# Optimization experiments

Measured on AMD Instinct MI355X. Metric: run time of the kernel, lower is better.

Reference implementation:

```python
import jax, jax.numpy as jnp
import numpy as np

E, T, A, H = 64, 128, 32, 4
S, O, QH1, QD, C1 = 256, 128, 128, 64, 128  # state, obs, query hidden, query/key dim, c hidden


def setup_inputs() -> dict:
    key = jax.random.key(0)
    ks = jax.random.split(key, 10)
    w = 0.02
    return {
        "q_values": jax.random.normal(ks[0], (E, T, A), jnp.float32),
        "states": jax.random.normal(ks[1], (E, T, S), jnp.float32),
        "individual_fs": jax.random.normal(ks[2], (E, T, A, O), jnp.float32),
        "Wq1": jax.random.normal(ks[3], (S, QH1), jnp.float32) * w,
        "bq1": jnp.zeros((QH1,), jnp.float32),
        "Wq2": jax.random.normal(ks[4], (QH1, QD), jnp.float32) * w,
        "bq2": jnp.zeros((QD,), jnp.float32),
        "Wk": jax.random.normal(ks[5], (H, O, QD), jnp.float32) * w,
        "bk": jnp.zeros((H, QD), jnp.float32),
        "Wc1": jax.random.normal(ks[6], (S, C1), jnp.float32) * w,
        "bc1": jnp.zeros((C1,), jnp.float32),
        "Wc2": jax.random.normal(ks[7], (C1, 1), jnp.float32) * w,
        "bc2": jnp.zeros((1,), jnp.float32),
    }


def reference(q_values, states, individual_fs, Wq1, bq1, Wq2, bq2, Wk, bk, Wc1, bc1, Wc2, bc2):
    e, t, a = q_values.shape
    s = states.reshape(-1, states.shape[-1])              # (B, S), B = E*T
    f = individual_fs.reshape(e * t, a, -1)               # (B, A, O)
    # query embedding of state: 2-layer MLP with ReLU
    emb_s = jnp.maximum(s @ Wq1 + bq1, 0.0) @ Wq2 + bq2   # (B, QD)
    # all-agents, all-heads key extraction in one batched einsum
    emb_u = jnp.einsum('bao,hok->bahk', f, Wk) + bk       # (B, A, H, QD)
    # query-key dot products per agent/head, then sum over heads
    Lambda_i = jnp.einsum('bk,bahk->bah', emb_s, emb_u).sum(axis=-1)  # (B, A)
    # state-dependent scalar bias
    c_value = jnp.maximum(s @ Wc1 + bc1, 0.0) @ Wc2 + bc2  # (B, 1)
    Q_tot = jnp.sum(Lambda_i * q_values.reshape(-1, a), axis=-1, keepdims=True) + c_value
    return Q_tot.reshape(e, t, 1)
```

## Files before the change

kernel.cpp:

```cpp
#include <hip/hip_runtime.h>


static constexpr int Sd  = 256;
static constexpr int Ad  = 32;
static constexpr int Od  = 128;
static constexpr int QDd = 64;
static constexpr int NB  = 16;
static constexpr int A_BLOCKS = 512;
static constexpr int B_BLOCKS = 1024;

__global__ void qatten_prep(const float* __restrict__ Wk, const float* __restrict__ bk,
                            float* __restrict__ WkT, float* __restrict__ bkSum)
{
    int idx = blockIdx.x * 256 + threadIdx.x;
    int k = idx >> 7;
    int o = idx & 127;
    float s = 0.f;
#pragma unroll
    for (int h = 0; h < 4; ++h) s += Wk[h * (Od * QDd) + o * QDd + k];
    WkT[k * Od + o] = s;
    if (idx < QDd) {
        float t = 0.f;
#pragma unroll
        for (int h = 0; h < 4; ++h) t += bk[h * QDd + idx];
        bkSum[idx] = t;
    }
}

__global__ __launch_bounds__(256, 4) void qatten_main(
    const float* __restrict__ qv, const float* __restrict__ st, const float* __restrict__ fs,
    const float* __restrict__ Wq1, const float* __restrict__ bq1,
    const float* __restrict__ Wq2, const float* __restrict__ bq2,
    const float* __restrict__ Wc1, const float* __restrict__ bc1,
    const float* __restrict__ Wc2, const float* __restrict__ bc2,
    const float* __restrict__ WkT, const float* __restrict__ bkSum,
    float* __restrict__ v_out, float* __restrict__ bias_out, float* __restrict__ g_out)
{
    __shared__ float s_lds[NB][Sd];
    __shared__ float h_lds[NB][260];
    __shared__ float emb_lds[NB][68];

    const int tid = threadIdx.x;
    const int bid = blockIdx.x;

    if (bid < A_BLOCKS) {
        const int b0 = bid * NB;

        {
            const float4* sp = (const float4*)(st + (size_t)b0 * Sd);
            float4* sl = (float4*)&s_lds[0][0];
            sl[tid]       = sp[tid];
            sl[tid + 256] = sp[tid + 256];
            sl[tid + 512] = sp[tid + 512];
            sl[tid + 768] = sp[tid + 768];
        }
        __syncthreads();

        {
            const int wg = tid & 63;
            const int rg = (tid >> 6) << 2;
            const float* __restrict__ Wb = (wg < 32) ? (Wq1 + 4 * wg)
                                                     : (Wc1 + 4 * (wg - 32));
            const float4 bb4 = (wg < 32) ? *(const float4*)&bq1[4 * wg]
                                         : *(const float4*)&bc1[4 * (wg - 32)];
            float acc[4][4];
#pragma unroll
            for (int r = 0; r < 4; ++r)
#pragma unroll
                for (int c = 0; c < 4; ++c) acc[r][c] = 0.f;

            for (int k = 0; k < Sd; k += 4) {
                float w[4][4], sv[4][4];
#pragma unroll
                for (int kk = 0; kk < 4; ++kk) {
                    const float4 t = *(const float4*)&Wb[(size_t)(k + kk) * 128];
                    w[kk][0] = t.x; w[kk][1] = t.y; w[kk][2] = t.z; w[kk][3] = t.w;
                }
#pragma unroll
                for (int r = 0; r < 4; ++r) {
                    const float4 t = *(const float4*)&s_lds[rg + r][k];
                    sv[r][0] = t.x; sv[r][1] = t.y; sv[r][2] = t.z; sv[r][3] = t.w;
                }
#pragma unroll
                for (int r = 0; r < 4; ++r)
#pragma unroll
                    for (int kk = 0; kk < 4; ++kk)
#pragma unroll
                        for (int c = 0; c < 4; ++c)
                            acc[r][c] = fmaf(sv[r][kk], w[kk][c], acc[r][c]);
            }
#pragma unroll
            for (int r = 0; r < 4; ++r) {
                float4 o;
                o.x = fmaxf(acc[r][0] + bb4.x, 0.f);
                o.y = fmaxf(acc[r][1] + bb4.y, 0.f);
                o.z = fmaxf(acc[r][2] + bb4.z, 0.f);
                o.w = fmaxf(acc[r][3] + bb4.w, 0.f);
                *(float4*)&h_lds[rg + r][4 * wg] = o;
            }
        }
        __syncthreads();

        {
            const int cg = tid & 15;
            const int row = tid >> 4;
            float acc[4] = {0.f, 0.f, 0.f, 0.f};
            for (int k = 0; k < 128; k += 4) {
                float w[4][4];
#pragma unroll
                for (int kk = 0; kk < 4; ++kk) {
                    const float4 t = *(const float4*)&Wq2[(size_t)(k + kk) * 64 + 4 * cg];
                    w[kk][0] = t.x; w[kk][1] = t.y; w[kk][2] = t.z; w[kk][3] = t.w;
                }
                const float4 h4 = *(const float4*)&h_lds[row][k];
                float hv[4] = {h4.x, h4.y, h4.z, h4.w};
#pragma unroll
                for (int kk = 0; kk < 4; ++kk)
#pragma unroll
                    for (int c = 0; c < 4; ++c)
                        acc[c] = fmaf(hv[kk], w[kk][c], acc[c]);
            }
            const float4 b4 = *(const float4*)&bq2[4 * cg];
            float4 o;
            o.x = acc[0] + b4.x; o.y = acc[1] + b4.y;
            o.z = acc[2] + b4.z; o.w = acc[3] + b4.w;
            *(float4*)&emb_lds[row][4 * cg] = o;
        }
        __syncthreads();

        {
            const int cg = tid & 31;
            const int rp = (tid >> 5) << 1;
            float acc[2][4];
#pragma unroll
            for (int r = 0; r < 2; ++r)
#pragma unroll
                for (int c = 0; c < 4; ++c) acc[r][c] = 0.f;
            for (int k = 0; k < QDd; k += 4) {
                float w[4][4], ev[2][4];
#pragma unroll
                for (int kk = 0; kk < 4; ++kk) {
                    const float4 t = *(const float4*)&WkT[(size_t)(k + kk) * 128 + 4 * cg];
                    w[kk][0] = t.x; w[kk][1] = t.y; w[kk][2] = t.z; w[kk][3] = t.w;
                }
#pragma unroll
                for (int r = 0; r < 2; ++r) {
                    const float4 t = *(const float4*)&emb_lds[rp + r][k];
                    ev[r][0] = t.x; ev[r][1] = t.y; ev[r][2] = t.z; ev[r][3] = t.w;
                }
#pragma unroll
                for (int r = 0; r < 2; ++r)
#pragma unroll
                    for (int kk = 0; kk < 4; ++kk)
#pragma unroll
                        for (int c = 0; c < 4; ++c)
                            acc[r][c] = fmaf(ev[r][kk], w[kk][c], acc[r][c]);
            }
#pragma unroll
            for (int r = 0; r < 2; ++r) {
                float4 o;
                o.x = acc[r][0]; o.y = acc[r][1]; o.z = acc[r][2]; o.w = acc[r][3];
                *(float4*)&v_out[(size_t)(b0 + rp + r) * Od + 4 * cg] = o;
            }
        }

        {
            const int b = tid >> 4;
            const int i = tid & 15;
            float pb = 0.f, pc = 0.f;
#pragma unroll
            for (int k = i; k < QDd; k += 16)  pb = fmaf(emb_lds[b][k], bkSum[k], pb);
#pragma unroll
            for (int j = i; j < 128; j += 16)  pc = fmaf(h_lds[b][128 + j], Wc2[j], pc);
            float pq = qv[(size_t)(b0 + b) * Ad + i] + qv[(size_t)(b0 + b) * Ad + i + 16];
#pragma unroll
            for (int d = 8; d >= 1; d >>= 1) {
                pb += __shfl_down(pb, d, 16);
                pc += __shfl_down(pc, d, 16);
                pq += __shfl_down(pq, d, 16);
            }
            if (i == 0) bias_out[b0 + b] = (pc + bc2[0]) + pb * pq;
        }
    } else {
        const int bidx = bid - A_BLOCKS;
        const int w = tid >> 6;
        const int l = tid & 63;
        const int r0 = bidx * 8 + w * 2;
        const float4* __restrict__ f0 = (const float4*)fs + (size_t)r0 * (Ad * Od / 4);
        const float4* __restrict__ f1 = f0 + (Ad * Od / 4);
        const float q0 = qv[(size_t)r0 * Ad + (l & 31)];
        const float q1 = qv[(size_t)(r0 + 1) * Ad + (l & 31)];
        float4 a0 = {0.f, 0.f, 0.f, 0.f}, a1 = {0.f, 0.f, 0.f, 0.f};
#pragma unroll
        for (int batch = 0; batch < 2; ++batch) {
            float4 x0[8], x1[8];
#pragma unroll
            for (int i = 0; i < 8; ++i) {
                x0[i] = f0[(batch * 8 + i) * 64 + l];
                x1[i] = f1[(batch * 8 + i) * 64 + l];
            }
#pragma unroll
            for (int i = 0; i < 8; ++i) {
                const int ii = batch * 8 + i;
                const float qa0 = __shfl(q0, 2 * ii + (l >> 5), 64);
                const float qa1 = __shfl(q1, 2 * ii + (l >> 5), 64);
                a0.x = fmaf(qa0, x0[i].x, a0.x);
                a0.y = fmaf(qa0, x0[i].y, a0.y);
                a0.z = fmaf(qa0, x0[i].z, a0.z);
                a0.w = fmaf(qa0, x0[i].w, a0.w);
                a1.x = fmaf(qa1, x1[i].x, a1.x);
                a1.y = fmaf(qa1, x1[i].y, a1.y);
                a1.z = fmaf(qa1, x1[i].z, a1.z);
                a1.w = fmaf(qa1, x1[i].w, a1.w);
            }
        }
        a0.x += __shfl_xor(a0.x, 32, 64);
        a0.y += __shfl_xor(a0.y, 32, 64);
        a0.z += __shfl_xor(a0.z, 32, 64);
        a0.w += __shfl_xor(a0.w, 32, 64);
        a1.x += __shfl_xor(a1.x, 32, 64);
        a1.y += __shfl_xor(a1.y, 32, 64);
        a1.z += __shfl_xor(a1.z, 32, 64);
        a1.w += __shfl_xor(a1.w, 32, 64);
        if (l < 32) {
            *(float4*)(g_out + (size_t)r0 * Od + l * 4) = a0;
            *(float4*)(g_out + (size_t)(r0 + 1) * Od + l * 4) = a1;
        }
    }
}

__global__ __launch_bounds__(256, 8) void qatten_final(
    const float* __restrict__ g, const float* __restrict__ v,
    const float* __restrict__ bias, float* __restrict__ out)
{
    const int tid = threadIdx.x;
    const int b = blockIdx.x * 8 + (tid >> 5);
    const int i = tid & 31;
    const float4 gv = *(const float4*)(g + (size_t)b * Od + i * 4);
    const float4 vv = *(const float4*)(v + (size_t)b * Od + i * 4);
    float d = gv.x * vv.x;
    d = fmaf(gv.y, vv.y, d);
    d = fmaf(gv.z, vv.z, d);
    d = fmaf(gv.w, vv.w, d);
#pragma unroll
    for (int k = 16; k >= 1; k >>= 1) d += __shfl_down(d, k, 32);
    if (i == 0) out[b] = d + bias[b];
}

extern "C" void kernel_launch(void* const* d_in, const int* in_sizes, int n_in,
                              void* d_out, int out_size, void* d_ws, size_t ws_size,
                              hipStream_t stream) {
    const float* qv  = (const float*)d_in[0];
    const float* st  = (const float*)d_in[1];
    const float* fs  = (const float*)d_in[2];
    const float* Wq1 = (const float*)d_in[3];
    const float* bq1 = (const float*)d_in[4];
    const float* Wq2 = (const float*)d_in[5];
    const float* bq2 = (const float*)d_in[6];
    const float* Wk  = (const float*)d_in[7];
    const float* bk  = (const float*)d_in[8];
    const float* Wc1 = (const float*)d_in[9];
    const float* bc1 = (const float*)d_in[10];
    const float* Wc2 = (const float*)d_in[11];
    const float* bc2 = (const float*)d_in[12];
    float* out = (float*)d_out;

    float* WkT   = (float*)d_ws;
    float* bkSum = WkT + QDd * Od;
    float* bias  = bkSum + QDd;
    float* vbuf  = bias + 8192;
    float* gbuf  = vbuf + 8192 * Od;

    qatten_prep<<<32, 256, 0, stream>>>(Wk, bk, WkT, bkSum);
    qatten_main<<<A_BLOCKS + B_BLOCKS, 256, 0, stream>>>(
        qv, st, fs, Wq1, bq1, Wq2, bq2, Wc1, bc1, Wc2, bc2,
        WkT, bkSum, vbuf, bias, gbuf);
    qatten_final<<<1024, 256, 0, stream>>>(gbuf, vbuf, bias, out);
}
```

Baseline: 241.8 us.

## Fuse streaming, MLP and final dot into one warp-specialized kernel

Merges the heterogeneous main kernel and the final reduction kernel into a single 512-thread block per 16 rows. Half the threads stream individual_fs and accumulate q-weighted features into shared memory while the other half compute the MLP chain; the final dot product and bias are then done in-block. This removes the global round trip for g, v and bias plus one kernel launch, and overlaps the feature stream with the MLP compute. In exchange there are fewer blocks (512), higher register pressure from prefetched float4 arrays, and serialized MLP phases in which only half the threads work.

```diff
diff --git a/kernel.cpp b/kernel.cpp
--- a/kernel.cpp
+++ b/kernel.cpp
@@ -6,8 +6,7 @@
 static constexpr int Od  = 128;
 static constexpr int QDd = 64;
 static constexpr int NB  = 16;
-static constexpr int A_BLOCKS = 512;
-static constexpr int B_BLOCKS = 1024;
+static constexpr int NBLK = 512;
 
 __global__ void qatten_prep(const float* __restrict__ Wk, const float* __restrict__ bk,
                             float* __restrict__ WkT, float* __restrict__ bkSum)
@@ -27,183 +26,84 @@
     }
 }
 
-__global__ __launch_bounds__(256, 4) void qatten_main(
+__global__ __launch_bounds__(512, 4) void qatten_fused(
     const float* __restrict__ qv, const float* __restrict__ st, const float* __restrict__ fs,
     const float* __restrict__ Wq1, const float* __restrict__ bq1,
     const float* __restrict__ Wq2, const float* __restrict__ bq2,
     const float* __restrict__ Wc1, const float* __restrict__ bc1,
     const float* __restrict__ Wc2, const float* __restrict__ bc2,
     const float* __restrict__ WkT, const float* __restrict__ bkSum,
-    float* __restrict__ v_out, float* __restrict__ bias_out, float* __restrict__ g_out)
+    float* __restrict__ out)
 {
     __shared__ float s_lds[NB][Sd];
     __shared__ float h_lds[NB][260];
     __shared__ float emb_lds[NB][68];
+    __shared__ float g_lds[NB][128];
 
     const int tid = threadIdx.x;
-    const int bid = blockIdx.x;
-
-    if (bid < A_BLOCKS) {
-        const int b0 = bid * NB;
-
+    const int b0 = blockIdx.x * NB;
+    const bool streamer = (tid < 256);
+    const int l = tid & 63;
+
+    float4 x0a[8], x1a[8];
+    float q0p0 = 0.f, q1p0 = 0.f, q0p1 = 0.f, q1p1 = 0.f;
+    const float4* f0p0 = nullptr;
+
+    if (streamer) {
+        const int w = tid >> 6;
+        const int rA0 = b0 + 4 * w;
+        f0p0 = (const float4*)fs + (size_t)rA0 * (Ad * Od / 4);
+        q0p0 = qv[(size_t)rA0 * Ad + (l & 31)];
+        q1p0 = qv[(size_t)(rA0 + 1) * Ad + (l & 31)];
+        q0p1 = qv[(size_t)(rA0 + 2) * Ad + (l & 31)];
+        q1p1 = qv[(size_t)(rA0 + 3) * Ad + (l & 31)];
+        const float4* __restrict__ f1 = f0p0 + (Ad * Od / 4);
+#pragma unroll
+        for (int i = 0; i < 8; ++i) {
+            x0a[i] = f0p0[i * 64 + l];
+            x1a[i] = f1[i * 64 + l];
+        }
+    } else {
+        const int t = tid - 256;
+        const float4* sp = (const float4*)(st + (size_t)b0 * Sd);
+        float4* sl = (float4*)&s_lds[0][0];
+        sl[t]       = sp[t];
+        sl[t + 256] = sp[t + 256];
+        sl[t + 512] = sp[t + 512];
+        sl[t + 768] = sp[t + 768];
+    }
+    __syncthreads();
+
+    if (streamer) {
+        const int w = tid >> 6;
+        const float4* __restrict__ f0 = f0p0;
+        const float4* __restrict__ f1 = f0 + (Ad * Od / 4);
+        float4 a0 = {0.f, 0.f, 0.f, 0.f}, a1 = {0.f, 0.f, 0.f, 0.f};
+#pragma unroll
+        for (int i = 0; i < 8; ++i) {
+            const float qa0 = __shfl(q0p0, 2 * i + (l >> 5), 64);
+            const float qa1 = __shfl(q1p0, 2 * i + (l >> 5), 64);
+            a0.x = fmaf(qa0, x0a[i].x, a0.x);
+            a0.y = fmaf(qa0, x0a[i].y, a0.y);
+            a0.z = fmaf(qa0, x0a[i].z, a0.z);
+            a0.w = fmaf(qa0, x0a[i].w, a0.w);
+            a1.x = fmaf(qa1, x1a[i].x, a1.x);
+            a1.y = fmaf(qa1, x1a[i].y, a1.y);
+            a1.z = fmaf(qa1, x1a[i].z, a1.z);
+            a1.w = fmaf(qa1, x1a[i].w, a1.w);
+        }
         {
-            const float4* sp = (const float4*)(st + (size_t)b0 * Sd);
-            float4* sl = (float4*)&s_lds[0][0];
-            sl[tid]       = sp[tid];
-            sl[tid + 256] = sp[tid + 256];
-            sl[tid + 512] = sp[tid + 512];
-            sl[tid + 768] = sp[tid + 768];
-        }
-        __syncthreads();
-
-        {
-            const int wg = tid & 63;
-            const int rg = (tid >> 6) << 2;
-            const float* __restrict__ Wb = (wg < 32) ? (Wq1 + 4 * wg)
-                                                     : (Wc1 + 4 * (wg - 32));
-            const float4 bb4 = (wg < 32) ? *(const float4*)&bq1[4 * wg]
-                                         : *(const float4*)&bc1[4 * (wg - 32)];
-            float acc[4][4];
-#pragma unroll
-            for (int r = 0; r < 4; ++r)
-#pragma unroll
-                for (int c = 0; c < 4; ++c) acc[r][c] = 0.f;
-
-            for (int k = 0; k < Sd; k += 4) {
-                float w[4][4], sv[4][4];
-#pragma unroll
-                for (int kk = 0; kk < 4; ++kk) {
-                    const float4 t = *(const float4*)&Wb[(size_t)(k + kk) * 128];
-                    w[kk][0] = t.x; w[kk][1] = t.y; w[kk][2] = t.z; w[kk][3] = t.w;
-                }
-#pragma unroll
-                for (int r = 0; r < 4; ++r) {
-                    const float4 t = *(const float4*)&s_lds[rg + r][k];
-                    sv[r][0] = t.x; sv[r][1] = t.y; sv[r][2] = t.z; sv[r][3] = t.w;
-                }
-#pragma unroll
-                for (int r = 0; r < 4; ++r)
-#pragma unroll
-                    for (int kk = 0; kk < 4; ++kk)
-#pragma unroll
-                        for (int c = 0; c < 4; ++c)
-                            acc[r][c] = fmaf(sv[r][kk], w[kk][c], acc[r][c]);
-            }
-#pragma unroll
-            for (int r = 0; r < 4; ++r) {
-                float4 o;
-                o.x = fmaxf(acc[r][0] + bb4.x, 0.f);
-                o.y = fmaxf(acc[r][1] + bb4.y, 0.f);
-                o.z = fmaxf(acc[r][2] + bb4.z, 0.f);
-                o.w = fmaxf(acc[r][3] + bb4.w, 0.f);
-                *(float4*)&h_lds[rg + r][4 * wg] = o;
-            }
-        }
-        __syncthreads();
-
-        {
-            const int cg = tid & 15;
-            const int row = tid >> 4;
-            float acc[4] = {0.f, 0.f, 0.f, 0.f};
-            for (int k = 0; k < 128; k += 4) {
-                float w[4][4];
-#pragma unroll
-                for (int kk = 0; kk < 4; ++kk) {
-                    const float4 t = *(const float4*)&Wq2[(size_t)(k + kk) * 64 + 4 * cg];
-                    w[kk][0] = t.x; w[kk][1] = t.y; w[kk][2] = t.z; w[kk][3] = t.w;
-                }
-                const float4 h4 = *(const float4*)&h_lds[row][k];
-                float hv[4] = {h4.x, h4.y, h4.z, h4.w};
-#pragma unroll
-                for (int kk = 0; kk < 4; ++kk)
-#pragma unroll
-                    for (int c = 0; c < 4; ++c)
-                        acc[c] = fmaf(hv[kk], w[kk][c], acc[c]);
-            }
-            const float4 b4 = *(const float4*)&bq2[4 * cg];
-            float4 o;
-            o.x = acc[0] + b4.x; o.y = acc[1] + b4.y;
-            o.z = acc[2] + b4.z; o.w = acc[3] + b4.w;
-            *(float4*)&emb_lds[row][4 * cg] = o;
-        }
-        __syncthreads();
-
-        {
-            const int cg = tid & 31;
-            const int rp = (tid >> 5) << 1;
-            float acc[2][4];
-#pragma unroll
-            for (int r = 0; r < 2; ++r)
-#pragma unroll
-                for (int c = 0; c < 4; ++c) acc[r][c] = 0.f;
-            for (int k = 0; k < QDd; k += 4) {
-                float w[4][4], ev[2][4];
-#pragma unroll
-                for (int kk = 0; kk < 4; ++kk) {
-                    const float4 t = *(const float4*)&WkT[(size_t)(k + kk) * 128 + 4 * cg];
-                    w[kk][0] = t.x; w[kk][1] = t.y; w[kk][2] = t.z; w[kk][3] = t.w;
-                }
-#pragma unroll
-                for (int r = 0; r < 2; ++r) {
-                    const float4 t = *(const float4*)&emb_lds[rp + r][k];
-                    ev[r][0] = t.x; ev[r][1] = t.y; ev[r][2] = t.z; ev[r][3] = t.w;
-                }
-#pragma unroll
-                for (int r = 0; r < 2; ++r)
-#pragma unroll
-                    for (int kk = 0; kk < 4; ++kk)
-#pragma unroll
-                        for (int c = 0; c < 4; ++c)
-                            acc[r][c] = fmaf(ev[r][kk], w[kk][c], acc[r][c]);
-            }
-#pragma unroll
-            for (int r = 0; r < 2; ++r) {
-                float4 o;
-                o.x = acc[r][0]; o.y = acc[r][1]; o.z = acc[r][2]; o.w = acc[r][3];
-                *(float4*)&v_out[(size_t)(b0 + rp + r) * Od + 4 * cg] = o;
-            }
-        }
-
-        {
-            const int b = tid >> 4;
-            const int i = tid & 15;
-            float pb = 0.f, pc = 0.f;
-#pragma unroll
-            for (int k = i; k < QDd; k += 16)  pb = fmaf(emb_lds[b][k], bkSum[k], pb);
-#pragma unroll
-            for (int j = i; j < 128; j += 16)  pc = fmaf(h_lds[b][128 + j], Wc2[j], pc);
-            float pq = qv[(size_t)(b0 + b) * Ad + i] + qv[(size_t)(b0 + b) * Ad + i + 16];
-#pragma unroll
-            for (int d = 8; d >= 1; d >>= 1) {
-                pb += __shfl_down(pb, d, 16);
-                pc += __shfl_down(pc, d, 16);
-                pq += __shfl_down(pq, d, 16);
-            }
-            if (i == 0) bias_out[b0 + b] = (pc + bc2[0]) + pb * pq;
-        }
-    } else {
-        const int bidx = bid - A_BLOCKS;
-        const int w = tid >> 6;
-        const int l = tid & 63;
-        const int r0 = bidx * 8 + w * 2;
-        const float4* __restrict__ f0 = (const float4*)fs + (size_t)r0 * (Ad * Od / 4);
-        const float4* __restrict__ f1 = f0 + (Ad * Od / 4);
-        const float q0 = qv[(size_t)r0 * Ad + (l & 31)];
-        const float q1 = qv[(size_t)(r0 + 1) * Ad + (l & 31)];
-        float4 a0 = {0.f, 0.f, 0.f, 0.f}, a1 = {0.f, 0.f, 0.f, 0.f};
-#pragma unroll
-        for (int batch = 0; batch < 2; ++batch) {
             float4 x0[8], x1[8];
 #pragma unroll
             for (int i = 0; i < 8; ++i) {
-                x0[i] = f0[(batch * 8 + i) * 64 + l];
-                x1[i] = f1[(batch * 8 + i) * 64 + l];
+                x0[i] = f0[(8 + i) * 64 + l];
+                x1[i] = f1[(8 + i) * 64 + l];
             }
 #pragma unroll
             for (int i = 0; i < 8; ++i) {
-                const int ii = batch * 8 + i;
-                const float qa0 = __shfl(q0, 2 * ii + (l >> 5), 64);
-                const float qa1 = __shfl(q1, 2 * ii + (l >> 5), 64);
+                const int ii = 8 + i;
+                const float qa0 = __shfl(q0p0, 2 * ii + (l >> 5), 64);
+                const float qa1 = __shfl(q1p0, 2 * ii + (l >> 5), 64);
                 a0.x = fmaf(qa0, x0[i].x, a0.x);
                 a0.y = fmaf(qa0, x0[i].y, a0.y);
                 a0.z = fmaf(qa0, x0[i].z, a0.z);
@@ -223,28 +123,180 @@
         a1.z += __shfl_xor(a1.z, 32, 64);
         a1.w += __shfl_xor(a1.w, 32, 64);
         if (l < 32) {
-            *(float4*)(g_out + (size_t)r0 * Od + l * 4) = a0;
-            *(float4*)(g_out + (size_t)(r0 + 1) * Od + l * 4) = a1;
-        }
-    }
-}
-
-__global__ __launch_bounds__(256, 8) void qatten_final(
-    const float* __restrict__ g, const float* __restrict__ v,
-    const float* __restrict__ bias, float* __restrict__ out)
-{
-    const int tid = threadIdx.x;
-    const int b = blockIdx.x * 8 + (tid >> 5);
-    const int i = tid & 31;
-    const float4 gv = *(const float4*)(g + (size_t)b * Od + i * 4);
-    const float4 vv = *(const float4*)(v + (size_t)b * Od + i * 4);
-    float d = gv.x * vv.x;
-    d = fmaf(gv.y, vv.y, d);
-    d = fmaf(gv.z, vv.z, d);
-    d = fmaf(gv.w, vv.w, d);
-#pragma unroll
-    for (int k = 16; k >= 1; k >>= 1) d += __shfl_down(d, k, 32);
-    if (i == 0) out[b] = d + bias[b];
+            *(float4*)&g_lds[4 * w][l * 4]     = a0;
+            *(float4*)&g_lds[4 * w + 1][l * 4] = a1;
+        }
+        const float4* __restrict__ g0 = f0 + 2 * (Ad * Od / 4);
+        const float4* __restrict__ g1 = f0 + 3 * (Ad * Od / 4);
+        float4 b0v = {0.f, 0.f, 0.f, 0.f}, b1v = {0.f, 0.f, 0.f, 0.f};
+#pragma unroll
+        for (int batch = 0; batch < 2; ++batch) {
+            float4 x0[8], x1[8];
+#pragma unroll
+            for (int i = 0; i < 8; ++i) {
+                x0[i] = g0[(batch * 8 + i) * 64 + l];
+                x1[i] = g1[(batch * 8 + i) * 64 + l];
+            }
+#pragma unroll
+            for (int i = 0; i < 8; ++i) {
+                const int ii = batch * 8 + i;
+                const float qa0 = __shfl(q0p1, 2 * ii + (l >> 5), 64);
+                const float qa1 = __shfl(q1p1, 2 * ii + (l >> 5), 64);
+                b0v.x = fmaf(qa0, x0[i].x, b0v.x);
+                b0v.y = fmaf(qa0, x0[i].y, b0v.y);
+                b0v.z = fmaf(qa0, x0[i].z, b0v.z);
+                b0v.w = fmaf(qa0, x0[i].w, b0v.w);
+                b1v.x = fmaf(qa1, x1[i].x, b1v.x);
+                b1v.y = fmaf(qa1, x1[i].y, b1v.y);
+                b1v.z = fmaf(qa1, x1[i].z, b1v.z);
+                b1v.w = fmaf(qa1, x1[i].w, b1v.w);
+            }
+        }
+        b0v.x += __shfl_xor(b0v.x, 32, 64);
+        b0v.y += __shfl_xor(b0v.y, 32, 64);
+        b0v.z += __shfl_xor(b0v.z, 32, 64);
+        b0v.w += __shfl_xor(b0v.w, 32, 64);
+        b1v.x += __shfl_xor(b1v.x, 32, 64);
+        b1v.y += __shfl_xor(b1v.y, 32, 64);
+        b1v.z += __shfl_xor(b1v.z, 32, 64);
+        b1v.w += __shfl_xor(b1v.w, 32, 64);
+        if (l < 32) {
+            *(float4*)&g_lds[4 * w + 2][l * 4] = b0v;
+            *(float4*)&g_lds[4 * w + 3][l * 4] = b1v;
+        }
+    } else {
+        const int t = tid - 256;
+        const int wg = t & 63;
+        const int rg = (t >> 6) << 2;
+        const float* __restrict__ Wb = (wg < 32) ? (Wq1 + 4 * wg)
+                                                 : (Wc1 + 4 * (wg - 32));
+        const float4 bb4 = (wg < 32) ? *(const float4*)&bq1[4 * wg]
+                                     : *(const float4*)&bc1[4 * (wg - 32)];
+        float acc[4][4];
+#pragma unroll
+        for (int r = 0; r < 4; ++r)
+#pragma unroll
+            for (int c = 0; c < 4; ++c) acc[r][c] = 0.f;
+
+        for (int k = 0; k < Sd; k += 4) {
+            float w[4][4], sv[4][4];
+#pragma unroll
+            for (int kk = 0; kk < 4; ++kk) {
+                const float4 tt = *(const float4*)&Wb[(size_t)(k + kk) * 128];
+                w[kk][0] = tt.x; w[kk][1] = tt.y; w[kk][2] = tt.z; w[kk][3] = tt.w;
+            }
+#pragma unroll
+            for (int r = 0; r < 4; ++r) {
+                const float4 tt = *(const float4*)&s_lds[rg + r][k];
+                sv[r][0] = tt.x; sv[r][1] = tt.y; sv[r][2] = tt.z; sv[r][3] = tt.w;
+            }
+#pragma unroll
+            for (int r = 0; r < 4; ++r)
+#pragma unroll
+                for (int kk = 0; kk < 4; ++kk)
+#pragma unroll
+                    for (int c = 0; c < 4; ++c)
+                        acc[r][c] = fmaf(sv[r][kk], w[kk][c], acc[r][c]);
+        }
+#pragma unroll
+        for (int r = 0; r < 4; ++r) {
+            float4 o;
+            o.x = fmaxf(acc[r][0] + bb4.x, 0.f);
+            o.y = fmaxf(acc[r][1] + bb4.y, 0.f);
+            o.z = fmaxf(acc[r][2] + bb4.z, 0.f);
+            o.w = fmaxf(acc[r][3] + bb4.w, 0.f);
+            *(float4*)&h_lds[rg + r][4 * wg] = o;
+        }
+    }
+    __syncthreads();
+
+    if (!streamer) {
+        const int t = tid - 256;
+        const int cg = t & 15;
+        const int row = t >> 4;
+        float acc[4] = {0.f, 0.f, 0.f, 0.f};
+        for (int k = 0; k < 128; k += 4) {
+            float w[4][4];
+#pragma unroll
+            for (int kk = 0; kk < 4; ++kk) {
+                const float4 tt = *(const float4*)&Wq2[(size_t)(k + kk) * 64 + 4 * cg];
+                w[kk][0] = tt.x; w[kk][1] = tt.y; w[kk][2] = tt.z; w[kk][3] = tt.w;
+            }
+            const float4 h4 = *(const float4*)&h_lds[row][k];
+#pragma unroll
+            for (int c = 0; c < 4; ++c) {
+                float a = acc[c];
+                a = fmaf(h4.x, w[0][c], a);
+                a = fmaf(h4.y, w[1][c], a);
+                a = fmaf(h4.z, w[2][c], a);
+                a = fmaf(h4.w, w[3][c], a);
+                acc[c] = a;
+            }
+        }
+        const float4 b4 = *(const float4*)&bq2[4 * cg];
+        float4 o;
+        o.x = acc[0] + b4.x; o.y = acc[1] + b4.y;
+        o.z = acc[2] + b4.z; o.w = acc[3] + b4.w;
+        *(float4*)&emb_lds[row][4 * cg] = o;
+    }
+    __syncthreads();
+
+    if (!streamer) {
+        const int t = tid - 256;
+        const int cg = t & 31;
+        const int rp = (t >> 5) << 1;
+        float acc[2][4];
+#pragma unroll
+        for (int r = 0; r < 2; ++r)
+#pragma unroll
+            for (int c = 0; c < 4; ++c) acc[r][c] = 0.f;
+        for (int k = 0; k < QDd; k += 4) {
+            float w[4][4], ev[2][4];
+#pragma unroll
+            for (int kk = 0; kk < 4; ++kk) {
+                const float4 tt = *(const float4*)&WkT[(size_t)(k + kk) * 128 + 4 * cg];
+                w[kk][0] = tt.x; w[kk][1] = tt.y; w[kk][2] = tt.z; w[kk][3] = tt.w;
+            }
+#pragma unroll
+            for (int r = 0; r < 2; ++r) {
+                const float4 tt = *(const float4*)&emb_lds[rp + r][k];
+                ev[r][0] = tt.x; ev[r][1] = tt.y; ev[r][2] = tt.z; ev[r][3] = tt.w;
+            }
+#pragma unroll
+            for (int r = 0; r < 2; ++r)
+#pragma unroll
+                for (int kk = 0; kk < 4; ++kk)
+#pragma unroll
+                    for (int c = 0; c < 4; ++c)
+                        acc[r][c] = fmaf(ev[r][kk], w[kk][c], acc[r][c]);
+        }
+#pragma unroll
+        for (int r = 0; r < 2; ++r) {
+            const int row = rp + r;
+            const int b = b0 + row;
+            const float4 g4 = *(const float4*)&g_lds[row][4 * cg];
+            float d = acc[r][0] * g4.x;
+            d = fmaf(acc[r][1], g4.y, d);
+            d = fmaf(acc[r][2], g4.z, d);
+            d = fmaf(acc[r][3], g4.w, d);
+            float pb = fmaf(emb_lds[row][cg],      bkSum[cg],      0.f);
+            pb       = fmaf(emb_lds[row][cg + 32], bkSum[cg + 32], pb);
+            float pc = 0.f;
+#pragma unroll
+            for (int j = 0; j < 4; ++j)
+                pc = fmaf(h_lds[row][128 + cg + 32 * j], Wc2[cg + 32 * j], pc);
+            float pq = qv[(size_t)b * Ad + cg];
+#pragma unroll
+            for (int dd = 16; dd >= 1; dd >>= 1) {
+                d  += __shfl_down(d,  dd, 32);
+                pb += __shfl_down(pb, dd, 32);
+                pc += __shfl_down(pc, dd, 32);
+                pq += __shfl_down(pq, dd, 32);
+            }
+            if (cg == 0)
+                out[b] = d + (pc + bc2[0]) + pb * pq;
+        }
+    }
 }
 
 extern "C" void kernel_launch(void* const* d_in, const int* in_sizes, int n_in,
@@ -267,13 +319,8 @@
 
     float* WkT   = (float*)d_ws;
     float* bkSum = WkT + QDd * Od;
-    float* bias  = bkSum + QDd;
-    float* vbuf  = bias + 8192;
-    float* gbuf  = vbuf + 8192 * Od;
 
     qatten_prep<<<32, 256, 0, stream>>>(Wk, bk, WkT, bkSum);
-    qatten_main<<<A_BLOCKS + B_BLOCKS, 256, 0, stream>>>(
-        qv, st, fs, Wq1, bq1, Wq2, bq2, Wc1, bc1, Wc2, bc2,
-        WkT, bkSum, vbuf, bias, gbuf);
-    qatten_final<<<1024, 256, 0, stream>>>(gbuf, vbuf, bias, out);
+    qatten_fused<<<NBLK, 512, 0, stream>>>(qv, st, fs, Wq1, bq1, Wq2, bq2,
+                                           Wc1, bc1, Wc2, bc2, WkT, bkSum, out);
 }
```

Result: slower. 281.6 us (+16.5%).
